# Optimization experiments

Measured on AMD Instinct MI355X. Metric: run time of the kernel, lower is better.

The kernel has to match this reference:

```python
import jax, jax.numpy as jnp
import numpy as np

B, T, C = 8, 2048, 1024   # batch, seq_len, n_embd
H = 128                   # head_size

def setup_inputs() -> dict:
    key = jax.random.key(0)
    kx, kk, kq, kv = jax.random.split(key, 4)
    scale = 1.0 / np.sqrt(C)
    return {
        "x": jax.random.normal(kx, (B, T, C), dtype=jnp.float32),
        "Wk": jax.random.normal(kk, (C, H), dtype=jnp.float32) * scale,
        "Wq": jax.random.normal(kq, (C, H), dtype=jnp.float32) * scale,
        "Wv": jax.random.normal(kv, (C, H), dtype=jnp.float32) * scale,
    }

def reference(x, Wk, Wq, Wv):
    # k,q,v: [B,T,H]
    k = x @ Wk
    q = x @ Wq
    v = x @ Wv
    # NOTE: original scales by C**-0.5 (n_embd), not head_size**-0.5
    wei = jnp.einsum("bth,bsh->bts", q, k) * (x.shape[-1] ** -0.5)  # [B,T,T]
    wei = jax.nn.softmax(wei, axis=-1)  # no causal mask in the source module
    # dropout = 0.0 -> identity
    out = jnp.einsum("bts,bsh->bth", wei, v)  # [B,T,H]
    return out
```

## Files before the change

### kernel.cpp

```cpp
#include <hip/hip_runtime.h>
#include <hip/hip_bf16.h>
#include <stdint.h>
#include <stddef.h>

#define NB 8
#define NT 2048
#define NC 1024
#define NH 128

typedef float f32x4 __attribute__((ext_vector_type(4)));
typedef short bf16x8 __attribute__((ext_vector_type(8)));

__device__ __forceinline__ unsigned short f2bf(float f) {
    union { float f; uint32_t u; } v; v.f = f;
    uint32_t u = v.u;
    u += 0x7fffu + ((u >> 16) & 1u);
    return (unsigned short)(u >> 16);
}

__device__ __forceinline__ void gld16(const void* gp, void* lp) {
    __builtin_amdgcn_global_load_lds(
        (const __attribute__((address_space(1))) unsigned int*)gp,
        (__attribute__((address_space(3))) unsigned int*)lp, 16, 0, 0);
}


__global__ __launch_bounds__(256) void cast_w_kernel(const float* __restrict__ Wq,
                                                     const float* __restrict__ Wk,
                                                     const float* __restrict__ Wv,
                                                     unsigned short* __restrict__ Wtf) {
    int gid  = blockIdx.x * 256 + threadIdx.x;
    int lane = gid & 63;
    int fs   = gid >> 6;
    int kb   = fs & 31;
    int g    = fs >> 5;
    int w    = g >> 3;
    int g16  = g & 7;
    int quad = lane >> 4;
    int l16  = lane & 15;
    const float* src = (w == 0) ? Wq : ((w == 1) ? Wk : Wv);
    int n = g16 * 16 + l16;
    bf16x8 o;
#pragma unroll
    for (int j = 0; j < 8; ++j)
        o[j] = (short)f2bf(src[(size_t)(kb * 32 + quad * 8 + j) * 128 + n]);
    *(bf16x8*)(Wtf + (size_t)gid * 8) = o;
}

#define XS_STRIDE 526
#define CS_STRIDE 398

__global__ __launch_bounds__(256, 1) void proj_kernel(const float* __restrict__ x,
                                                      const unsigned short* __restrict__ Wtf,
                                                      unsigned short* __restrict__ Qf,
                                                      unsigned short* __restrict__ Kf,
                                                      unsigned short* __restrict__ Vf) {
    __shared__ __align__(16) unsigned short xs[64 * XS_STRIDE];
    __shared__ __align__(16) unsigned short wbuf[2][24 * 512];

    const int tid  = threadIdx.x;
    const int wave = tid >> 6;
    const int lane = tid & 63;
    const int quad = lane >> 4;
    const int l16  = lane & 15;
    const int bidx = blockIdx.x;
    const int rowbase = bidx * 64;
    const int b    = bidx >> 5;
    const int ib   = bidx & 31;

    auto stageX = [&](int phase) {
#pragma unroll
        for (int i = 0; i < 16; ++i) {
            const int row = i * 4 + wave;
            const int k   = lane * 8;
            const float* src = x + (size_t)(rowbase + row) * NC + phase * 512 + k;
            float4 f0 = *(const float4*)src;
            float4 f1 = *(const float4*)(src + 4);
            bf16x8 o;
            o[0] = (short)f2bf(f0.x); o[1] = (short)f2bf(f0.y);
            o[2] = (short)f2bf(f0.z); o[3] = (short)f2bf(f0.w);
            o[4] = (short)f2bf(f1.x); o[5] = (short)f2bf(f1.y);
            o[6] = (short)f2bf(f1.z); o[7] = (short)f2bf(f1.w);
            *(bf16x8*)(&xs[row * XS_STRIDE + k]) = o;
        }
    };
    auto stageW = [&](int kb, int bi) {
#pragma unroll
        for (int i = 0; i < 6; ++i) {
            const int g = wave * 6 + i;
            gld16(Wtf + ((size_t)(g * 32 + kb) * 512) + lane * 8, &wbuf[bi][g * 512]);
        }
    };

    stageX(0);
    stageW(0, 0);
    __syncthreads();

    f32x4 acc[24] = {};
    for (int kb = 0; kb < 32; ++kb) {
        const int cur = kb & 1;
        if (kb == 16) stageX(1);
        if (kb < 31) stageW(kb + 1, cur ^ 1);
        if (kb == 16) __syncthreads();
        const int kofs = (kb & 15) * 32 + quad * 8;
        bf16x8 a = *(const bf16x8*)(&xs[(wave * 16 + l16) * XS_STRIDE + kofs]);
#pragma unroll
        for (int g = 0; g < 24; ++g) {
            bf16x8 wf = *(const bf16x8*)(&wbuf[cur][g * 512 + lane * 8]);
            acc[g] = __builtin_amdgcn_mfma_f32_16x16x32_bf16(a, wf, acc[g], 0, 0, 0);
        }
        __syncthreads();
    }

    unsigned short* cs = xs;
#pragma unroll
    for (int g = 0; g < 24; ++g) {
#pragma unroll
        for (int r = 0; r < 4; ++r)
            cs[(wave * 16 + quad * 4 + r) * CS_STRIDE + g * 16 + l16] = f2bf(acc[g][r]);
    }
    __syncthreads();

    const int iq  = ib * 4 + wave;
    unsigned short* qdst = Qf + (size_t)b * (NT * NH);
    unsigned short* kdst = Kf + (size_t)b * (NT * NH);
    unsigned short* vdst = Vf + (size_t)b * (NT * NH);
#pragma unroll
    for (int ks = 0; ks < 4; ++ks) {
        bf16x8 vq = *(const bf16x8*)(&cs[(wave * 16 + l16) * CS_STRIDE + ks * 32 + quad * 8]);
        *(bf16x8*)(qdst + ((size_t)(iq * 4 + ks) * 64 + lane) * 8) = vq;
        bf16x8 vk = *(const bf16x8*)(&cs[(wave * 16 + l16) * CS_STRIDE + 128 + ks * 32 + quad * 8]);
        *(bf16x8*)(kdst + ((size_t)(iq * 4 + ks) * 64 + lane) * 8) = vk;
    }
    const int tc0 = ib * 2;
    const int c   = wave >> 1;
#pragma unroll
    for (int i = 0; i < 4; ++i) {
        const int nt = (wave & 1) * 4 + i;
        bf16x8 v;
#pragma unroll
        for (int j = 0; j < 8; ++j)
            v[j] = (short)cs[(c * 32 + quad * 8 + j) * CS_STRIDE + 256 + nt * 16 + l16];
        *(bf16x8*)(vdst + ((size_t)(nt * 64 + tc0 + c) * 64 + lane) * 8) = v;
    }
}

__global__ __launch_bounds__(256, 1) void attn_kernel(const unsigned short* __restrict__ Qf,
                                                      const unsigned short* __restrict__ Kf,
                                                      const unsigned short* __restrict__ Vf,
                                                      float* __restrict__ out) {
    __shared__ __align__(16) unsigned short kbuf[2][32 * 512];
    __shared__ __align__(16) unsigned short vbuf[2][32 * 512];
    __shared__ __align__(16) unsigned short p_all[4][16 * 136];

    const int tid  = threadIdx.x;
    const int wave = tid >> 6;
    const int lane = tid & 63;
    const int quad = lane >> 4;
    const int l16  = lane & 15;
    const int bid  = blockIdx.x;
    const int b    = bid & 7;
    const int iqb  = bid >> 3;
    const int iq   = iqb * 4 + wave;

    const unsigned short* qfp = Qf + (size_t)b * (NT * NH);
    const unsigned short* kfp = Kf + (size_t)b * (NT * NH);
    const unsigned short* vfp = Vf + (size_t)b * (NT * NH);
    unsigned short* p_w = p_all[wave];

    bf16x8 qf[4];
#pragma unroll
    for (int ks = 0; ks < 4; ++ks)
        qf[ks] = *(const bf16x8*)(qfp + ((size_t)(iq * 4 + ks) * 64 + lane) * 8);

    auto stage = [&](int kv, int bi) {
        const unsigned short* gk = kfp + ((size_t)(kv * 32 + wave * 8) * 512) + lane * 8;
#pragma unroll
        for (int i = 0; i < 8; ++i)
            gld16(gk + (size_t)i * 512, &kbuf[bi][(wave * 8 + i) * 512]);
#pragma unroll
        for (int i = 0; i < 8; ++i) {
            const int nt = wave * 2 + (i >> 2);
            const int k2 = i & 3;
            gld16(vfp + ((size_t)(nt * 64 + kv * 4 + k2) * 512) + lane * 8,
                  &vbuf[bi][(nt * 4 + k2) * 512]);
        }
    };

    stage(0, 0);
    __syncthreads();

    f32x4 O[8] = {};
    float lsum[4] = {0.f, 0.f, 0.f, 0.f};
    const float scl2 = 0.03125f * 1.44269504088896340736f;

    for (int kv = 0; kv < 16; ++kv) {
        const int cur = kv & 1;
        if (kv < 15) stage(kv + 1, cur ^ 1);

        f32x4 S[8] = {};
#pragma unroll
        for (int ks = 0; ks < 4; ++ks) {
            bf16x8 kf[8];
#pragma unroll
            for (int nt = 0; nt < 8; ++nt)
                kf[nt] = *(const bf16x8*)(&kbuf[cur][(nt * 4 + ks) * 512 + lane * 8]);
#pragma unroll
            for (int nt = 0; nt < 8; ++nt)
                S[nt] = __builtin_amdgcn_mfma_f32_16x16x32_bf16(qf[ks], kf[nt], S[nt], 0, 0, 0);
        }

#pragma unroll
        for (int nt = 0; nt < 8; ++nt) {
#pragma unroll
            for (int r = 0; r < 4; ++r) {
                float p = __builtin_amdgcn_exp2f(S[nt][r] * scl2);
                lsum[r] += p;
                p_w[(quad * 4 + r) * 136 + nt * 16 + l16] = f2bf(p);
            }
        }

#pragma unroll
        for (int k2 = 0; k2 < 4; ++k2) {
            bf16x8 vf[8];
#pragma unroll
            for (int nt = 0; nt < 8; ++nt)
                vf[nt] = *(const bf16x8*)(&vbuf[cur][(nt * 4 + k2) * 512 + lane * 8]);
            bf16x8 pf = *(const bf16x8*)(&p_w[l16 * 136 + k2 * 32 + quad * 8]);
#pragma unroll
            for (int nt = 0; nt < 8; ++nt)
                O[nt] = __builtin_amdgcn_mfma_f32_16x16x32_bf16(pf, vf[nt], O[nt], 0, 0, 0);
        }

        __syncthreads();
    }

#pragma unroll
    for (int msk = 1; msk <= 8; msk <<= 1) {
#pragma unroll
        for (int r = 0; r < 4; ++r)
            lsum[r] += __shfl_xor(lsum[r], msk, 64);
    }
    float inv[4];
#pragma unroll
    for (int r = 0; r < 4; ++r)
        inv[r] = 1.0f / lsum[r];
    float* orow = out + ((size_t)b * NT + iq * 16) * NH;
#pragma unroll
    for (int nt = 0; nt < 8; ++nt) {
#pragma unroll
        for (int r = 0; r < 4; ++r)
            orow[(quad * 4 + r) * NH + nt * 16 + l16] = O[nt][r] * inv[r];
    }
}

extern "C" void kernel_launch(void* const* d_in, const int* in_sizes, int n_in,
                              void* d_out, int out_size, void* d_ws, size_t ws_size,
                              hipStream_t stream) {
    const float* x  = (const float*)d_in[0];
    const float* Wk = (const float*)d_in[1];
    const float* Wq = (const float*)d_in[2];
    const float* Wv = (const float*)d_in[3];
    float* out = (float*)d_out;

    char* ws = (char*)d_ws;
    unsigned short* Qf  = (unsigned short*)(ws);
    unsigned short* Kf  = (unsigned short*)(ws + 4194304);
    unsigned short* Vf  = (unsigned short*)(ws + 8388608);
    unsigned short* Wtf = (unsigned short*)(ws + 12582912);

    cast_w_kernel<<<192, 256, 0, stream>>>(Wq, Wk, Wv, Wtf);
    proj_kernel<<<256, 256, 0, stream>>>(x, Wtf, Qf, Kf, Vf);
    attn_kernel<<<256, 256, 0, stream>>>(Qf, Kf, Vf, out);
}
```

Measured before the change: 177.8 us.

## Halve per-block tiles and split KV across waves to double grid size

The projection kernel now handles 32 rows per block. Each wave owns one 16-row tile and half of the 384 output columns, and it reads and casts x straight from global memory instead of staging it in LDS. The attention kernel now handles 32 queries per block with two waves per query tile, each taking half of every 32-key chunk. The two halves' O and row sums are combined through LDS at the end. Both grids grow from 256 to 512 blocks with launch bounds allowing 2 blocks per CU, to use more of the CUs. The cost is redundant K/V staging per query, more barriers per unit of work, and an extra LDS reduction.

```diff
diff --git a/kernel.cpp b/kernel.cpp
--- a/kernel.cpp
+++ b/kernel.cpp
@@ -47,15 +47,13 @@
     *(bf16x8*)(Wtf + (size_t)gid * 8) = o;
 }
 
-#define XS_STRIDE 526
-#define CS_STRIDE 398
-
-__global__ __launch_bounds__(256, 1) void proj_kernel(const float* __restrict__ x,
+#define CS2 392
+
+__global__ __launch_bounds__(256, 2) void proj_kernel(const float* __restrict__ x,
                                                       const unsigned short* __restrict__ Wtf,
                                                       unsigned short* __restrict__ Qf,
                                                       unsigned short* __restrict__ Kf,
                                                       unsigned short* __restrict__ Vf) {
-    __shared__ __align__(16) unsigned short xs[64 * XS_STRIDE];
     __shared__ __align__(16) unsigned short wbuf[2][24 * 512];
 
     const int tid  = threadIdx.x;
@@ -64,26 +62,13 @@
     const int quad = lane >> 4;
     const int l16  = lane & 15;
     const int bidx = blockIdx.x;
-    const int rowbase = bidx * 64;
-    const int b    = bidx >> 5;
-    const int ib   = bidx & 31;
-
-    auto stageX = [&](int phase) {
-#pragma unroll
-        for (int i = 0; i < 16; ++i) {
-            const int row = i * 4 + wave;
-            const int k   = lane * 8;
-            const float* src = x + (size_t)(rowbase + row) * NC + phase * 512 + k;
-            float4 f0 = *(const float4*)src;
-            float4 f1 = *(const float4*)(src + 4);
-            bf16x8 o;
-            o[0] = (short)f2bf(f0.x); o[1] = (short)f2bf(f0.y);
-            o[2] = (short)f2bf(f0.z); o[3] = (short)f2bf(f0.w);
-            o[4] = (short)f2bf(f1.x); o[5] = (short)f2bf(f1.y);
-            o[6] = (short)f2bf(f1.z); o[7] = (short)f2bf(f1.w);
-            *(bf16x8*)(&xs[row * XS_STRIDE + k]) = o;
-        }
-    };
+    const int rowbase = bidx * 32;
+    const int b    = bidx >> 6;
+    const int mt   = wave & 1;
+    const int nh   = wave >> 1;
+
+    const float* xrow = x + (size_t)(rowbase + mt * 16 + l16) * NC;
+
     auto stageW = [&](int kb, int bi) {
 #pragma unroll
         for (int i = 0; i < 6; ++i) {
@@ -92,66 +77,76 @@
         }
     };
 
-    stageX(0);
     stageW(0, 0);
     __syncthreads();
 
-    f32x4 acc[24] = {};
+    f32x4 acc[12] = {};
     for (int kb = 0; kb < 32; ++kb) {
         const int cur = kb & 1;
-        if (kb == 16) stageX(1);
         if (kb < 31) stageW(kb + 1, cur ^ 1);
-        if (kb == 16) __syncthreads();
-        const int kofs = (kb & 15) * 32 + quad * 8;
-        bf16x8 a = *(const bf16x8*)(&xs[(wave * 16 + l16) * XS_STRIDE + kofs]);
-#pragma unroll
-        for (int g = 0; g < 24; ++g) {
-            bf16x8 wf = *(const bf16x8*)(&wbuf[cur][g * 512 + lane * 8]);
-            acc[g] = __builtin_amdgcn_mfma_f32_16x16x32_bf16(a, wf, acc[g], 0, 0, 0);
+        const float* src = xrow + kb * 32 + quad * 8;
+        float4 f0 = *(const float4*)src;
+        float4 f1 = *(const float4*)(src + 4);
+        bf16x8 a;
+        a[0] = (short)f2bf(f0.x); a[1] = (short)f2bf(f0.y);
+        a[2] = (short)f2bf(f0.z); a[3] = (short)f2bf(f0.w);
+        a[4] = (short)f2bf(f1.x); a[5] = (short)f2bf(f1.y);
+        a[6] = (short)f2bf(f1.z); a[7] = (short)f2bf(f1.w);
+#pragma unroll
+        for (int i = 0; i < 12; ++i) {
+            bf16x8 wf = *(const bf16x8*)(&wbuf[cur][(nh * 12 + i) * 512 + lane * 8]);
+            acc[i] = __builtin_amdgcn_mfma_f32_16x16x32_bf16(a, wf, acc[i], 0, 0, 0);
         }
         __syncthreads();
     }
 
-    unsigned short* cs = xs;
-#pragma unroll
-    for (int g = 0; g < 24; ++g) {
-#pragma unroll
-        for (int r = 0; r < 4; ++r)
-            cs[(wave * 16 + quad * 4 + r) * CS_STRIDE + g * 16 + l16] = f2bf(acc[g][r]);
-    }
-    __syncthreads();
-
-    const int iq  = ib * 4 + wave;
+    unsigned short* cs = (unsigned short*)wbuf;
+#pragma unroll
+    for (int i = 0; i < 12; ++i) {
+        const int g = nh * 12 + i;
+#pragma unroll
+        for (int r = 0; r < 4; ++r)
+            cs[(mt * 16 + quad * 4 + r) * CS2 + g * 16 + l16] = f2bf(acc[i][r]);
+    }
+    __syncthreads();
+
+    const int ibase = (rowbase & (NT - 1)) >> 4;
+    const int tc    = (rowbase & (NT - 1)) >> 5;
     unsigned short* qdst = Qf + (size_t)b * (NT * NH);
     unsigned short* kdst = Kf + (size_t)b * (NT * NH);
     unsigned short* vdst = Vf + (size_t)b * (NT * NH);
-#pragma unroll
-    for (int ks = 0; ks < 4; ++ks) {
-        bf16x8 vq = *(const bf16x8*)(&cs[(wave * 16 + l16) * CS_STRIDE + ks * 32 + quad * 8]);
-        *(bf16x8*)(qdst + ((size_t)(iq * 4 + ks) * 64 + lane) * 8) = vq;
-        bf16x8 vk = *(const bf16x8*)(&cs[(wave * 16 + l16) * CS_STRIDE + 128 + ks * 32 + quad * 8]);
-        *(bf16x8*)(kdst + ((size_t)(iq * 4 + ks) * 64 + lane) * 8) = vk;
-    }
-    const int tc0 = ib * 2;
-    const int c   = wave >> 1;
-#pragma unroll
-    for (int i = 0; i < 4; ++i) {
-        const int nt = (wave & 1) * 4 + i;
+
+    {
+        const int mq   = wave & 1;
+        const int isK  = wave >> 1;
+        unsigned short* dst = isK ? kdst : qdst;
+        const int off = isK * 128;
+        const int iqt = ibase + mq;
+#pragma unroll
+        for (int ks = 0; ks < 4; ++ks) {
+            bf16x8 v = *(const bf16x8*)(&cs[(mq * 16 + l16) * CS2 + off + ks * 32 + quad * 8]);
+            *(bf16x8*)(dst + ((size_t)(iqt * 4 + ks) * 64 + lane) * 8) = v;
+        }
+    }
+#pragma unroll
+    for (int i = 0; i < 2; ++i) {
+        const int nt = wave * 2 + i;
         bf16x8 v;
 #pragma unroll
         for (int j = 0; j < 8; ++j)
-            v[j] = (short)cs[(c * 32 + quad * 8 + j) * CS_STRIDE + 256 + nt * 16 + l16];
-        *(bf16x8*)(vdst + ((size_t)(nt * 64 + tc0 + c) * 64 + lane) * 8) = v;
-    }
-}
-
-__global__ __launch_bounds__(256, 1) void attn_kernel(const unsigned short* __restrict__ Qf,
+            v[j] = (short)cs[(quad * 8 + j) * CS2 + 256 + nt * 16 + l16];
+        *(bf16x8*)(vdst + ((size_t)(nt * 64 + tc) * 64 + lane) * 8) = v;
+    }
+}
+
+__global__ __launch_bounds__(256, 2) void attn_kernel(const unsigned short* __restrict__ Qf,
                                                       const unsigned short* __restrict__ Kf,
                                                       const unsigned short* __restrict__ Vf,
                                                       float* __restrict__ out) {
-    __shared__ __align__(16) unsigned short kbuf[2][32 * 512];
-    __shared__ __align__(16) unsigned short vbuf[2][32 * 512];
-    __shared__ __align__(16) unsigned short p_all[4][16 * 136];
+    __shared__ __align__(16) unsigned short kbuf[2][16 * 512];
+    __shared__ __align__(16) unsigned short vbuf[2][16 * 512];
+    __shared__ __align__(16) unsigned short p_all[4][16 * 40];
+    __shared__ float sl[4][16];
 
     const int tid  = threadIdx.x;
     const int wave = tid >> 6;
@@ -161,7 +156,9 @@
     const int bid  = blockIdx.x;
     const int b    = bid & 7;
     const int iqb  = bid >> 3;
-    const int iq   = iqb * 4 + wave;
+    const int mt   = wave & 1;
+    const int kh   = wave >> 1;
+    const int iq   = iqb * 2 + mt;
 
     const unsigned short* qfp = Qf + (size_t)b * (NT * NH);
     const unsigned short* kfp = Kf + (size_t)b * (NT * NH);
@@ -173,17 +170,18 @@
     for (int ks = 0; ks < 4; ++ks)
         qf[ks] = *(const bf16x8*)(qfp + ((size_t)(iq * 4 + ks) * 64 + lane) * 8);
 
-    auto stage = [&](int kv, int bi) {
-        const unsigned short* gk = kfp + ((size_t)(kv * 32 + wave * 8) * 512) + lane * 8;
-#pragma unroll
-        for (int i = 0; i < 8; ++i)
-            gld16(gk + (size_t)i * 512, &kbuf[bi][(wave * 8 + i) * 512]);
+    auto stage = [&](int j, int bi) {
 #pragma unroll
         for (int i = 0; i < 8; ++i) {
-            const int nt = wave * 2 + (i >> 2);
-            const int k2 = i & 3;
-            gld16(vfp + ((size_t)(nt * 64 + kv * 4 + k2) * 512) + lane * 8,
-                  &vbuf[bi][(nt * 4 + k2) * 512]);
+            const int fid = wave * 8 + i;
+            if (fid < 16) {
+                gld16(kfp + ((size_t)(j * 16 + fid) * 512) + lane * 8, &kbuf[bi][fid * 512]);
+            } else {
+                const int s  = fid - 16;
+                const int nt = s >> 1;
+                const int c  = s & 1;
+                gld16(vfp + ((size_t)(nt * 64 + j * 2 + c) * 512) + lane * 8, &vbuf[bi][s * 512]);
+            }
         }
     };
 
@@ -194,63 +192,76 @@
     float lsum[4] = {0.f, 0.f, 0.f, 0.f};
     const float scl2 = 0.03125f * 1.44269504088896340736f;
 
-    for (int kv = 0; kv < 16; ++kv) {
-        const int cur = kv & 1;
-        if (kv < 15) stage(kv + 1, cur ^ 1);
-
-        f32x4 S[8] = {};
+    for (int j = 0; j < 32; ++j) {
+        const int cur = j & 1;
+        if (j < 31) stage(j + 1, cur ^ 1);
+
+        f32x4 S[2] = {};
 #pragma unroll
         for (int ks = 0; ks < 4; ++ks) {
-            bf16x8 kf[8];
-#pragma unroll
-            for (int nt = 0; nt < 8; ++nt)
-                kf[nt] = *(const bf16x8*)(&kbuf[cur][(nt * 4 + ks) * 512 + lane * 8]);
-#pragma unroll
-            for (int nt = 0; nt < 8; ++nt)
-                S[nt] = __builtin_amdgcn_mfma_f32_16x16x32_bf16(qf[ks], kf[nt], S[nt], 0, 0, 0);
-        }
-
+            bf16x8 kf0 = *(const bf16x8*)(&kbuf[cur][((kh * 2 + 0) * 4 + ks) * 512 + lane * 8]);
+            bf16x8 kf1 = *(const bf16x8*)(&kbuf[cur][((kh * 2 + 1) * 4 + ks) * 512 + lane * 8]);
+            S[0] = __builtin_amdgcn_mfma_f32_16x16x32_bf16(qf[ks], kf0, S[0], 0, 0, 0);
+            S[1] = __builtin_amdgcn_mfma_f32_16x16x32_bf16(qf[ks], kf1, S[1], 0, 0, 0);
+        }
+
+#pragma unroll
+        for (int n2 = 0; n2 < 2; ++n2) {
+#pragma unroll
+            for (int r = 0; r < 4; ++r) {
+                float p = __builtin_amdgcn_exp2f(S[n2][r] * scl2);
+                lsum[r] += p;
+                p_w[(quad * 4 + r) * 40 + n2 * 16 + l16] = f2bf(p);
+            }
+        }
+
+        bf16x8 pf = *(const bf16x8*)(&p_w[l16 * 40 + quad * 8]);
 #pragma unroll
         for (int nt = 0; nt < 8; ++nt) {
+            bf16x8 vf = *(const bf16x8*)(&vbuf[cur][(nt * 2 + kh) * 512 + lane * 8]);
+            O[nt] = __builtin_amdgcn_mfma_f32_16x16x32_bf16(pf, vf, O[nt], 0, 0, 0);
+        }
+
+        __syncthreads();
+    }
+
+#pragma unroll
+    for (int msk = 1; msk <= 8; msk <<= 1) {
+#pragma unroll
+        for (int r = 0; r < 4; ++r)
+            lsum[r] += __shfl_xor(lsum[r], msk, 64);
+    }
+
+    if (l16 == 0) {
+#pragma unroll
+        for (int r = 0; r < 4; ++r)
+            sl[wave][quad * 4 + r] = lsum[r];
+    }
+    float* so = (float*)kbuf;
+    if (wave >= 2) {
+#pragma unroll
+        for (int nt = 0; nt < 8; ++nt) {
+#pragma unroll
+            for (int r = 0; r < 4; ++r)
+                so[((size_t)(wave - 2) * 16 + quad * 4 + r) * 132 + nt * 16 + l16] = O[nt][r];
+        }
+    }
+    __syncthreads();
+
+    if (wave < 2) {
+        float inv[4];
+#pragma unroll
+        for (int r = 0; r < 4; ++r)
+            inv[r] = 1.0f / (sl[wave][quad * 4 + r] + sl[wave + 2][quad * 4 + r]);
+        float* orow = out + ((size_t)b * NT + iq * 16) * NH;
+#pragma unroll
+        for (int nt = 0; nt < 8; ++nt) {
 #pragma unroll
             for (int r = 0; r < 4; ++r) {
-                float p = __builtin_amdgcn_exp2f(S[nt][r] * scl2);
-                lsum[r] += p;
-                p_w[(quad * 4 + r) * 136 + nt * 16 + l16] = f2bf(p);
+                float v = O[nt][r] + so[((size_t)wave * 16 + quad * 4 + r) * 132 + nt * 16 + l16];
+                orow[(quad * 4 + r) * NH + nt * 16 + l16] = v * inv[r];
             }
         }
-
-#pragma unroll
-        for (int k2 = 0; k2 < 4; ++k2) {
-            bf16x8 vf[8];
-#pragma unroll
-            for (int nt = 0; nt < 8; ++nt)
-                vf[nt] = *(const bf16x8*)(&vbuf[cur][(nt * 4 + k2) * 512 + lane * 8]);
-            bf16x8 pf = *(const bf16x8*)(&p_w[l16 * 136 + k2 * 32 + quad * 8]);
-#pragma unroll
-            for (int nt = 0; nt < 8; ++nt)
-                O[nt] = __builtin_amdgcn_mfma_f32_16x16x32_bf16(pf, vf[nt], O[nt], 0, 0, 0);
-        }
-
-        __syncthreads();
-    }
-
-#pragma unroll
-    for (int msk = 1; msk <= 8; msk <<= 1) {
-#pragma unroll
-        for (int r = 0; r < 4; ++r)
-            lsum[r] += __shfl_xor(lsum[r], msk, 64);
-    }
-    float inv[4];
-#pragma unroll
-    for (int r = 0; r < 4; ++r)
-        inv[r] = 1.0f / lsum[r];
-    float* orow = out + ((size_t)b * NT + iq * 16) * NH;
-#pragma unroll
-    for (int nt = 0; nt < 8; ++nt) {
-#pragma unroll
-        for (int r = 0; r < 4; ++r)
-            orow[(quad * 4 + r) * NH + nt * 16 + l16] = O[nt][r] * inv[r];
     }
 }
 
@@ -270,6 +281,6 @@
     unsigned short* Wtf = (unsigned short*)(ws + 12582912);
 
     cast_w_kernel<<<192, 256, 0, stream>>>(Wq, Wk, Wv, Wtf);
-    proj_kernel<<<256, 256, 0, stream>>>(x, Wtf, Qf, Kf, Vf);
-    attn_kernel<<<256, 256, 0, stream>>>(Qf, Kf, Vf, out);
-}
+    proj_kernel<<<512, 256, 0, stream>>>(x, Wtf, Qf, Kf, Vf);
+    attn_kernel<<<512, 256, 0, stream>>>(Qf, Kf, Vf, out);
+}
```

After: 176.9 us. No clear change (-0.5%).
